# Kernel tuning notes

Measured on AMD Instinct MI355X. Metric: run time of the kernel, lower is better.

Reference implementation:

```python
import jax, jax.numpy as jnp
import numpy as np

D_MODEL = 1024
NUM_HEADS = 16
D_K = D_MODEL // NUM_HEADS
THETA = 10000.0


def _apply_rope(x, positions):
    # x: [B, H, S, d_k], positions: [B, S]
    dk = x.shape[-1]
    freq = 1.0 / (THETA ** (jnp.arange(0, dk, 2, dtype=jnp.float32) / dk))  # [dk/2]
    ang = positions.astype(jnp.float32)[:, None, :, None] * freq  # [B,1,S,dk/2]
    cos, sin = jnp.cos(ang), jnp.sin(ang)
    x_even = x[..., 0::2]
    x_odd = x[..., 1::2]
    re = x_even * cos - x_odd * sin
    ro = x_even * sin + x_odd * cos
    # interleave back: [..., dk/2, 2] -> [..., dk]
    return jnp.stack([re, ro], axis=-1).reshape(x.shape)


def setup_inputs() -> dict:
    key = jax.random.key(0)
    kx, kq, kk, kv, ko = jax.random.split(key, 5)
    B, S = 2, 2048
    std = (2.0 / (D_MODEL + D_MODEL)) ** 0.5
    x = jax.random.normal(kx, (B, S, D_MODEL), dtype=jnp.float32)
    Wq = jax.random.normal(kq, (D_MODEL, D_MODEL), dtype=jnp.float32) * std
    Wk = jax.random.normal(kk, (D_MODEL, D_MODEL), dtype=jnp.float32) * std
    Wv = jax.random.normal(kv, (D_MODEL, D_MODEL), dtype=jnp.float32) * std
    Wo = jax.random.normal(ko, (D_MODEL, D_MODEL), dtype=jnp.float32) * std
    token_positions = jnp.tile(jnp.arange(S, dtype=jnp.int32)[None, :], (B, 1))
    return {"x": x, "Wq": Wq, "Wk": Wk, "Wv": Wv, "Wo": Wo,
            "token_positions": token_positions}


def reference(x, Wq, Wk, Wv, Wo, token_positions):
    B, S, D = x.shape
    H, dk = NUM_HEADS, D_K
    scale = 1.0 / np.sqrt(dk)
    # Linear is y = x @ W.T with W:[d_out, d_in]
    q = jnp.einsum('bsd,ed->bse', x, Wq).reshape(B, S, H, dk).transpose(0, 2, 1, 3)
    k = jnp.einsum('bsd,ed->bse', x, Wk).reshape(B, S, H, dk).transpose(0, 2, 1, 3)
    v = jnp.einsum('bsd,ed->bse', x, Wv).reshape(B, S, H, dk).transpose(0, 2, 1, 3)
    q = _apply_rope(q, token_positions)
    k = _apply_rope(k, token_positions)
    scores = jnp.einsum('bhqd,bhkd->bhqk', q, k) * scale  # [B,H,S,S]
    causal = jnp.tril(jnp.ones((S, S), dtype=bool))
    scores = jnp.where(causal[None, None, :, :], scores, -jnp.inf)
    probs = jax.nn.softmax(scores, axis=-1)
    attn = jnp.einsum('bhqk,bhkd->bhqd', probs, v)  # [B,H,S,dk]
    attn = attn.transpose(0, 2, 1, 3).reshape(B, S, D)
    return jnp.einsum('bsd,ed->bse', attn, Wo)
```

## Files before the change

kernel.cpp:

```cpp
#include <hip/hip_runtime.h>
#include <hip/hip_bf16.h>
#include <math.h>

#define B_  2
#define S_  2048
#define H_  16
#define D_  1024
#define DK_ 64

typedef __attribute__((ext_vector_type(8))) short bf16x8;
typedef __attribute__((ext_vector_type(8))) unsigned short ushort8v;
typedef __attribute__((ext_vector_type(4))) float f32x4;

__device__ __forceinline__ unsigned short f2bf(float f) {
  unsigned u = __float_as_uint(f);
  unsigned r = (u + 0x7FFFu + ((u >> 16) & 1u)) >> 16;
  return (unsigned short)r;
}
__device__ __forceinline__ unsigned pack_trunc(float lo, float hi) {
  return (__float_as_uint(lo) >> 16) | (__float_as_uint(hi) & 0xffff0000u);
}
__device__ __forceinline__ float fast_exp2(float x) {
#if __has_builtin(__builtin_amdgcn_exp2f)
  return __builtin_amdgcn_exp2f(x);
#else
  return __expf(x * 0.69314718056f);
#endif
}
__device__ __forceinline__ void gload_lds16(const unsigned short* g,
                                            unsigned short* l) {
  __builtin_amdgcn_global_load_lds(
      (const __attribute__((address_space(1))) unsigned int*)(const void*)g,
      (__attribute__((address_space(3))) unsigned int*)(void*)l, 16, 0, 0);
}

__global__ __launch_bounds__(256)
void cast5_bf16(const float* __restrict__ x,  const float* __restrict__ wq,
                const float* __restrict__ wk, const float* __restrict__ wv,
                const float* __restrict__ wo,
                unsigned short* __restrict__ xb,  unsigned short* __restrict__ wqb,
                unsigned short* __restrict__ wkb, unsigned short* __restrict__ wvb,
                unsigned short* __restrict__ wob)
{
  const int idx = blockIdx.x;
  const float* s; unsigned short* d; int lblk;
  if (idx < 2048) { s = x; d = xb; lblk = idx; }
  else {
    int t = idx - 2048;
    int w = t >> 9;
    lblk  = t & 511;
    s = (w == 0) ? wq  : (w == 1) ? wk  : (w == 2) ? wv  : wo;
    d = (w == 0) ? wqb : (w == 1) ? wkb : (w == 2) ? wvb : wob;
  }
  size_t i0 = ((size_t)lblk * 256 + threadIdx.x) * 8;
  float4 v0 = *(const float4*)(s + i0);
  float4 v1 = *(const float4*)(s + i0 + 4);
  ushort8v o;
  o[0] = f2bf(v0.x); o[1] = f2bf(v0.y); o[2] = f2bf(v0.z); o[3] = f2bf(v0.w);
  o[4] = f2bf(v1.x); o[5] = f2bf(v1.y); o[6] = f2bf(v1.z); o[7] = f2bf(v1.w);
  *(ushort8v*)(d + i0) = o;
}

__global__ __launch_bounds__(256)
void gemm_qkv(const unsigned short* __restrict__ A0,
              const unsigned short* __restrict__ W0,
              const unsigned short* __restrict__ W1,
              const unsigned short* __restrict__ W2,
              unsigned short* __restrict__ qh,
              unsigned short* __restrict__ kh,
              unsigned short* __restrict__ vt,
              const int* __restrict__ tp)
{
  const int z = blockIdx.z;

  __shared__ unsigned short As[128 * 32];
  __shared__ unsigned short Bs[128 * 32];
  __shared__ int tps[128];

  const int tid   = threadIdx.x;
  const int wave  = tid >> 6;
  const int lane  = tid & 63;
  const int quad  = lane >> 4;
  const int col16 = lane & 15;
  const int wr    = (wave >> 1) * 64;
  const int wc    = (wave & 1) * 64;

  const int row0 = (z == 2) ? blockIdx.x * 128 : blockIdx.y * 128;
  const int col0 = (z == 2) ? blockIdx.y * 128 : blockIdx.x * 128;
  const unsigned short* Aptr = (z == 0) ? A0 : (z == 1) ? A0 : W2;
  const unsigned short* Bptr = (z == 0) ? W0 : (z == 1) ? W1 : A0;

  if (z < 2 && tid < 128) tps[tid] = tp[row0 + tid];

  const int srow = wave * 16 + (lane >> 2);
  const int scol = ((lane & 3) ^ ((lane >> 2) & 3)) * 8;
  const unsigned short* gA = Aptr + (size_t)(row0 + srow) * D_ + scol;
  const unsigned short* gB = Bptr + (size_t)(col0 + srow) * D_ + scol;
  unsigned short* lA0 = &As[(wave * 16) * 32];
  unsigned short* lA1 = &As[(wave * 16 + 64) * 32];
  unsigned short* lB0 = &Bs[(wave * 16) * 32];
  unsigned short* lB1 = &Bs[(wave * 16 + 64) * 32];

  f32x4 acc[4][4];
  #pragma unroll
  for (int mt = 0; mt < 4; ++mt)
    #pragma unroll
    for (int nt = 0; nt < 4; ++nt)
      #pragma unroll
      for (int r = 0; r < 4; ++r) acc[mt][nt][r] = 0.f;

  const int jx = (quad ^ (col16 & 3)) * 8;

  for (int k0 = 0; k0 < D_; k0 += 32) {
    __syncthreads();
    gload_lds16(gA + k0,                   lA0);
    gload_lds16(gA + (size_t)64 * D_ + k0, lA1);
    gload_lds16(gB + k0,                   lB0);
    gload_lds16(gB + (size_t)64 * D_ + k0, lB1);
    __syncthreads();

    bf16x8 af[4], bfr[4];
    #pragma unroll
    for (int mt = 0; mt < 4; ++mt)
      af[mt] = *(const bf16x8*)&As[(wr + mt * 16 + col16) * 32 + jx];
    #pragma unroll
    for (int nt = 0; nt < 4; ++nt)
      bfr[nt] = *(const bf16x8*)&Bs[(wc + nt * 16 + col16) * 32 + jx];

    #pragma unroll
    for (int mt = 0; mt < 4; ++mt)
      #pragma unroll
      for (int nt = 0; nt < 4; ++nt)
        acc[mt][nt] = __builtin_amdgcn_mfma_f32_16x16x32_bf16(
            af[mt], bfr[nt], acc[mt][nt], 0, 0, 0);
  }

  if (z == 2) {
    #pragma unroll
    for (int mt = 0; mt < 4; ++mt)
      #pragma unroll
      for (int r = 0; r < 4; ++r) {
        int c = row0 + wr + mt * 16 + quad * 4 + r;
        int h = c >> 6, d = c & 63;
        #pragma unroll
        for (int nt = 0; nt < 4; ++nt) {
          int t  = col0 + wc + nt * 16 + col16;
          int bb = t >> 11, sl = t & (S_ - 1);
          vt[((size_t)((bb << 4) + h) * DK_ + d) * S_ + sl] =
              f2bf(acc[mt][nt][r]);
        }
      }
  } else {
    unsigned short* C = z ? kh : qh;
    const float qs = z ? 1.0f : 0.1803368801111204f;
    const float sgn = (col16 & 1) ? 1.f : -1.f;
    float freqr[4];
    #pragma unroll
    for (int nt = 0; nt < 4; ++nt) {
      int i = ((wc + nt * 16 + col16) & 63) >> 1;
      freqr[nt] = exp2f(-0.4152410118f * (float)i);
    }
    #pragma unroll
    for (int mt = 0; mt < 4; ++mt)
      #pragma unroll
      for (int r = 0; r < 4; ++r) {
        int rl  = wr + mt * 16 + quad * 4 + r;
        int row = row0 + rl;
        float p = (float)tps[rl];
        #pragma unroll
        for (int nt = 0; nt < 4; ++nt) {
          int col = col0 + wc + nt * 16 + col16;
          float ang = p * freqr[nt];
          float sn = __sinf(ang), cs = __cosf(ang);
          float val = acc[mt][nt][r];
          float oth = __shfl_xor(val, 1);
          C[(size_t)row * D_ + col] = f2bf((val * cs + oth * sgn * sn) * qs);
        }
      }
  }
}

__global__ __launch_bounds__(256)
void gemm_wo(const unsigned short* __restrict__ A,
             const unsigned short* __restrict__ W,
             float* __restrict__ C)
{
  __shared__ unsigned short As[64 * 32];
  __shared__ unsigned short Bs[128 * 32];

  const int tid   = threadIdx.x;
  const int wave  = tid >> 6;
  const int lane  = tid & 63;
  const int quad  = lane >> 4;
  const int col16 = lane & 15;
  const int row0  = blockIdx.y * 64;
  const int col0  = blockIdx.x * 128;
  const int wr    = (wave >> 1) * 32;
  const int wc    = (wave & 1) * 64;

  const int srow = wave * 16 + (lane >> 2);
  const int scol = ((lane & 3) ^ ((lane >> 2) & 3)) * 8;
  const unsigned short* gA = A + (size_t)(row0 + srow) * D_ + scol;
  const unsigned short* gB = W + (size_t)(col0 + srow) * D_ + scol;
  unsigned short* lA0 = &As[(wave * 16) * 32];
  unsigned short* lB0 = &Bs[(wave * 16) * 32];
  unsigned short* lB1 = &Bs[(wave * 16 + 64) * 32];

  f32x4 acc[2][4];
  #pragma unroll
  for (int mt = 0; mt < 2; ++mt)
    #pragma unroll
    for (int nt = 0; nt < 4; ++nt)
      #pragma unroll
      for (int r = 0; r < 4; ++r) acc[mt][nt][r] = 0.f;

  const int jx = (quad ^ (col16 & 3)) * 8;

  for (int k0 = 0; k0 < D_; k0 += 32) {
    __syncthreads();
    gload_lds16(gA + k0,                   lA0);
    gload_lds16(gB + k0,                   lB0);
    gload_lds16(gB + (size_t)64 * D_ + k0, lB1);
    __syncthreads();

    bf16x8 af[2], bfr[4];
    #pragma unroll
    for (int mt = 0; mt < 2; ++mt)
      af[mt] = *(const bf16x8*)&As[(wr + mt * 16 + col16) * 32 + jx];
    #pragma unroll
    for (int nt = 0; nt < 4; ++nt)
      bfr[nt] = *(const bf16x8*)&Bs[(wc + nt * 16 + col16) * 32 + jx];

    #pragma unroll
    for (int mt = 0; mt < 2; ++mt)
      #pragma unroll
      for (int nt = 0; nt < 4; ++nt)
        acc[mt][nt] = __builtin_amdgcn_mfma_f32_16x16x32_bf16(
            af[mt], bfr[nt], acc[mt][nt], 0, 0, 0);
  }

  #pragma unroll
  for (int mt = 0; mt < 2; ++mt)
    #pragma unroll
    for (int r = 0; r < 4; ++r) {
      int row = row0 + wr + mt * 16 + quad * 4 + r;
      #pragma unroll
      for (int nt = 0; nt < 4; ++nt) {
        int col = col0 + wc + nt * 16 + col16;
        C[(size_t)row * D_ + col] = acc[mt][nt][r];
      }
    }
}

__device__ __forceinline__ void attn_side(
    const unsigned short* __restrict__ Ks, const unsigned short* __restrict__ Vs,
    unsigned short (* __restrict__ Pl)[72],
    const bf16x8* qf, f32x4* Oacc, float& l_i,
    int quad, int col, int qlocal, bool diag)
{
  const int jx = quad ^ (col & 7);
  f32x4 st[4];
  #pragma unroll
  for (int nb = 0; nb < 4; ++nb) {
    const int s0 = (nb * 16 + col) * 8 + jx;
    bf16x8 ka0 = *(const bf16x8*)(Ks + s0 * 8);
    bf16x8 ka1 = *(const bf16x8*)(Ks + (s0 ^ 4) * 8);
    f32x4 a = {-24.f, -24.f, -24.f, -24.f};
    a = __builtin_amdgcn_mfma_f32_16x16x32_bf16(ka0, qf[0], a, 0, 0, 0);
    a = __builtin_amdgcn_mfma_f32_16x16x32_bf16(ka1, qf[1], a, 0, 0, 0);
    st[nb] = a;
  }

  if (diag) {
    #pragma unroll
    for (int nb = 0; nb < 4; ++nb)
      #pragma unroll
      for (int r = 0; r < 4; ++r)
        if (nb * 16 + quad * 4 + r > qlocal) st[nb][r] = -1e30f;
  }

  float rsum = 0.f;
  #pragma unroll
  for (int nb = 0; nb < 4; ++nb)
    #pragma unroll
    for (int r = 0; r < 4; ++r) {
      float pv = fast_exp2(st[nb][r]);
      st[nb][r] = pv;
      rsum += pv;
    }
  rsum += __shfl_xor(rsum, 16);
  rsum += __shfl_xor(rsum, 32);
  l_i += rsum;

  #pragma unroll
  for (int nb = 0; nb < 4; ++nb) {
    uint2 pk;
    pk.x = pack_trunc(st[nb][0], st[nb][1]);
    pk.y = pack_trunc(st[nb][2], st[nb][3]);
    *(uint2*)&Pl[col][nb * 16 + quad * 4] = pk;
  }

  bf16x8 pf0 = *(const bf16x8*)&Pl[col][quad * 8];
  bf16x8 pf1 = *(const bf16x8*)&Pl[col][32 + quad * 8];
  #pragma unroll
  for (int nb = 0; nb < 4; ++nb) {
    const int s0 = (nb * 16 + col) * 8 + jx;
    bf16x8 va0 = *(const bf16x8*)(Vs + s0 * 8);
    bf16x8 va1 = *(const bf16x8*)(Vs + (s0 ^ 4) * 8);
    Oacc[nb] = __builtin_amdgcn_mfma_f32_16x16x32_bf16(va0, pf0, Oacc[nb], 0, 0, 0);
    Oacc[nb] = __builtin_amdgcn_mfma_f32_16x16x32_bf16(va1, pf1, Oacc[nb], 0, 0, 0);
  }
}

__global__ __launch_bounds__(256)
void attn_mfma(const unsigned short* __restrict__ Q,
               const unsigned short* __restrict__ K,
               const unsigned short* __restrict__ Vt,
               unsigned short* __restrict__ O)
{
  const int qtA  = blockIdx.x;
  const int qtB  = 31 - qtA;
  const int bh   = blockIdx.y;
  const int b    = bh >> 4, h = bh & 15;
  const int tid  = threadIdx.x;
  const int wave = tid >> 6;
  const int lane = tid & 63;
  const int quad = lane >> 4;
  const int col  = lane & 15;
  const int qlocal = wave * 16 + col;

  __shared__ unsigned short Ks[1024 * 8];
  __shared__ unsigned short Vs[1024 * 8];
  __shared__ unsigned short PlA[4][16][72];
  __shared__ unsigned short PlB[4][16][72];

  const size_t qkbase = (size_t)b * S_ * D_ + (size_t)h * DK_;
  const size_t vtbase = (size_t)bh * DK_ * S_;

  const int qrowA = qtA * 64 + qlocal;
  const int qrowB = qtB * 64 + qlocal;
  bf16x8 qfA[2], qfB[2];
  qfA[0] = *(const bf16x8*)(Q + qkbase + (size_t)qrowA * D_ + quad * 8);
  qfA[1] = *(const bf16x8*)(Q + qkbase + (size_t)qrowA * D_ + 32 + quad * 8);
  qfB[0] = *(const bf16x8*)(Q + qkbase + (size_t)qrowB * D_ + quad * 8);
  qfB[1] = *(const bf16x8*)(Q + qkbase + (size_t)qrowB * D_ + 32 + quad * 8);

  const int sr = tid >> 3;
  const int sj = (tid & 7) ^ (sr & 7);
  const unsigned short* gK = K + qkbase + (size_t)sr * D_ + sj * 8;
  const unsigned short* gV = Vt + vtbase + (size_t)sr * S_ + sj * 8;

  f32x4 OaccA[4], OaccB[4];
  #pragma unroll
  for (int nb = 0; nb < 4; ++nb)
    #pragma unroll
    for (int r = 0; r < 4; ++r) { OaccA[nb][r] = 0.f; OaccB[nb][r] = 0.f; }
  float lA = 0.f, lB = 0.f;

  const int nK128 = (qtB + 2) >> 1;

  for (int m = 0; m < nK128; ++m) {
    __syncthreads();
    #pragma unroll
    for (int half = 0; half < 2; ++half) {
      const int kbase = m * 128 + half * 64;
      #pragma unroll
      for (int p = 0; p < 2; ++p) {
        gload_lds16(gK + (size_t)(kbase + p * 32) * D_,
                    &Ks[(size_t)half * 4096 + (size_t)(p * 256 + wave * 64) * 8]);
        gload_lds16(gV + (size_t)(p * 32) * S_ + kbase,
                    &Vs[(size_t)half * 4096 + (size_t)(p * 256 + wave * 64) * 8]);
      }
    }
    __syncthreads();

    #pragma unroll
    for (int half = 0; half < 2; ++half) {
      const int g = 2 * m + half;
      const unsigned short* KsH = Ks + half * 4096;
      const unsigned short* VsH = Vs + half * 4096;
      if (g <= qtB)
        attn_side(KsH, VsH, PlB[wave], qfB, OaccB, lB, quad, col, qlocal,
                  g == qtB);
      if (g <= qtA)
        attn_side(KsH, VsH, PlA[wave], qfA, OaccA, lA, quad, col, qlocal,
                  g == qtA);
    }
  }

  const float invA = 1.0f / lA;
  const float invB = 1.0f / lB;
  #pragma unroll
  for (int nb = 0; nb < 4; ++nb) {
    int d = nb * 16 + quad * 4;
    ushort4 oa, ob;
    oa.x = f2bf(OaccA[nb][0] * invA); oa.y = f2bf(OaccA[nb][1] * invA);
    oa.z = f2bf(OaccA[nb][2] * invA); oa.w = f2bf(OaccA[nb][3] * invA);
    ob.x = f2bf(OaccB[nb][0] * invB); ob.y = f2bf(OaccB[nb][1] * invB);
    ob.z = f2bf(OaccB[nb][2] * invB); ob.w = f2bf(OaccB[nb][3] * invB);
    *(ushort4*)(O + (size_t)b * S_ * D_ + (size_t)qrowA * D_ + h * DK_ + d) = oa;
    *(ushort4*)(O + (size_t)b * S_ * D_ + (size_t)qrowB * D_ + h * DK_ + d) = ob;
  }
}

extern "C" void kernel_launch(void* const* d_in, const int* in_sizes, int n_in,
                              void* d_out, int out_size, void* d_ws, size_t ws_size,
                              hipStream_t stream)
{
  const float* x  = (const float*)d_in[0];
  const float* Wq = (const float*)d_in[1];
  const float* Wk = (const float*)d_in[2];
  const float* Wv = (const float*)d_in[3];
  const float* Wo = (const float*)d_in[4];
  const int*   tp = (const int*)d_in[5];
  float* out = (float*)d_out;

  const size_t NTOK = (size_t)B_ * S_ * D_;
  const size_t NW   = (size_t)D_ * D_;
  unsigned short* qh  = (unsigned short*)d_ws;
  unsigned short* kh  = qh + NTOK;
  unsigned short* vt  = kh + NTOK;
  unsigned short* xb  = vt + NTOK;
  unsigned short* wqb = xb + NTOK;
  unsigned short* wkb = wqb + NW;
  unsigned short* wvb = wkb + NW;
  unsigned short* wob = wvb + NW;
  unsigned short* ab  = xb;

  cast5_bf16<<<dim3(4096), 256, 0, stream>>>(
      x, Wq, Wk, Wv, Wo, xb, wqb, wkb, wvb, wob);

  gemm_qkv<<<dim3(D_ / 128, (B_ * S_) / 128, 3), 256, 0, stream>>>(
      xb, wqb, wkb, wvb, qh, kh, vt, tp);

  attn_mfma<<<dim3(16, B_ * H_), 256, 0, stream>>>(qh, kh, vt, ab);

  gemm_wo<<<dim3(D_ / 128, (B_ * S_) / 64), 256, 0, stream>>>(ab, wob, out);
}
```

Measured before the change: 192.4 us.

## Double-buffer LDS tiles in GEMM and attention loops, MFMA softmax row sums

The QKV GEMM, output GEMM and attention kernels now use two LDS buffers. Each loop prefetches the next K tile into the alternate buffer after one barrier per step, so the global-to-LDS copy overlaps the MFMA work on the current tile, and the second barrier is gone. The attention loop now steps through 64-key tiles instead of 128-key pairs. The softmax denominator is computed with an MFMA of the bf16 probability tile against a ones vector, replacing the per-lane adds and cross-lane shuffles. This uses more LDS in the GEMMs, which may reduce occupancy, and the row sum now uses bf16-rounded probabilities, which matches the numerator.

```diff
diff --git a/kernel.cpp b/kernel.cpp
--- a/kernel.cpp
+++ b/kernel.cpp
@@ -73,8 +73,8 @@
 {
   const int z = blockIdx.z;
 
-  __shared__ unsigned short As[128 * 32];
-  __shared__ unsigned short Bs[128 * 32];
+  __shared__ unsigned short As[2 * 128 * 32];
+  __shared__ unsigned short Bs[2 * 128 * 32];
   __shared__ int tps[128];
 
   const int tid   = threadIdx.x;
@@ -87,7 +87,7 @@
 
   const int row0 = (z == 2) ? blockIdx.x * 128 : blockIdx.y * 128;
   const int col0 = (z == 2) ? blockIdx.y * 128 : blockIdx.x * 128;
-  const unsigned short* Aptr = (z == 0) ? A0 : (z == 1) ? A0 : W2;
+  const unsigned short* Aptr = (z == 2) ? W2 : A0;
   const unsigned short* Bptr = (z == 0) ? W0 : (z == 1) ? W1 : A0;
 
   if (z < 2 && tid < 128) tps[tid] = tp[row0 + tid];
@@ -96,10 +96,15 @@
   const int scol = ((lane & 3) ^ ((lane >> 2) & 3)) * 8;
   const unsigned short* gA = Aptr + (size_t)(row0 + srow) * D_ + scol;
   const unsigned short* gB = Bptr + (size_t)(col0 + srow) * D_ + scol;
-  unsigned short* lA0 = &As[(wave * 16) * 32];
-  unsigned short* lA1 = &As[(wave * 16 + 64) * 32];
-  unsigned short* lB0 = &Bs[(wave * 16) * 32];
-  unsigned short* lB1 = &Bs[(wave * 16 + 64) * 32];
+
+  auto stage = [&](int k0, int buf) {
+    unsigned short* a = As + buf * 4096;
+    unsigned short* b = Bs + buf * 4096;
+    gload_lds16(gA + k0,                   a + (wave * 16) * 32);
+    gload_lds16(gA + (size_t)64 * D_ + k0, a + (wave * 16 + 64) * 32);
+    gload_lds16(gB + k0,                   b + (wave * 16) * 32);
+    gload_lds16(gB + (size_t)64 * D_ + k0, b + (wave * 16 + 64) * 32);
+  };
 
   f32x4 acc[4][4];
   #pragma unroll
@@ -111,21 +116,21 @@
 
   const int jx = (quad ^ (col16 & 3)) * 8;
 
+  stage(0, 0);
   for (int k0 = 0; k0 < D_; k0 += 32) {
+    const int buf = (k0 >> 5) & 1;
     __syncthreads();
-    gload_lds16(gA + k0,                   lA0);
-    gload_lds16(gA + (size_t)64 * D_ + k0, lA1);
-    gload_lds16(gB + k0,                   lB0);
-    gload_lds16(gB + (size_t)64 * D_ + k0, lB1);
-    __syncthreads();
-
+    if (k0 + 32 < D_) stage(k0 + 32, buf ^ 1);
+
+    const unsigned short* a = As + buf * 4096;
+    const unsigned short* b = Bs + buf * 4096;
     bf16x8 af[4], bfr[4];
     #pragma unroll
     for (int mt = 0; mt < 4; ++mt)
-      af[mt] = *(const bf16x8*)&As[(wr + mt * 16 + col16) * 32 + jx];
+      af[mt] = *(const bf16x8*)&a[(wr + mt * 16 + col16) * 32 + jx];
     #pragma unroll
     for (int nt = 0; nt < 4; ++nt)
-      bfr[nt] = *(const bf16x8*)&Bs[(wc + nt * 16 + col16) * 32 + jx];
+      bfr[nt] = *(const bf16x8*)&b[(wc + nt * 16 + col16) * 32 + jx];
 
     #pragma unroll
     for (int mt = 0; mt < 4; ++mt)
@@ -185,8 +190,8 @@
              const unsigned short* __restrict__ W,
              float* __restrict__ C)
 {
-  __shared__ unsigned short As[64 * 32];
-  __shared__ unsigned short Bs[128 * 32];
+  __shared__ unsigned short As[2 * 64 * 32];
+  __shared__ unsigned short Bs[2 * 128 * 32];
 
   const int tid   = threadIdx.x;
   const int wave  = tid >> 6;
@@ -202,9 +207,14 @@
   const int scol = ((lane & 3) ^ ((lane >> 2) & 3)) * 8;
   const unsigned short* gA = A + (size_t)(row0 + srow) * D_ + scol;
   const unsigned short* gB = W + (size_t)(col0 + srow) * D_ + scol;
-  unsigned short* lA0 = &As[(wave * 16) * 32];
-  unsigned short* lB0 = &Bs[(wave * 16) * 32];
-  unsigned short* lB1 = &Bs[(wave * 16 + 64) * 32];
+
+  auto stage = [&](int k0, int buf) {
+    unsigned short* a = As + buf * 2048;
+    unsigned short* b = Bs + buf * 4096;
+    gload_lds16(gA + k0,                   a + (wave * 16) * 32);
+    gload_lds16(gB + k0,                   b + (wave * 16) * 32);
+    gload_lds16(gB + (size_t)64 * D_ + k0, b + (wave * 16 + 64) * 32);
+  };
 
   f32x4 acc[2][4];
   #pragma unroll
@@ -216,20 +226,21 @@
 
   const int jx = (quad ^ (col16 & 3)) * 8;
 
+  stage(0, 0);
   for (int k0 = 0; k0 < D_; k0 += 32) {
+    const int buf = (k0 >> 5) & 1;
     __syncthreads();
-    gload_lds16(gA + k0,                   lA0);
-    gload_lds16(gB + k0,                   lB0);
-    gload_lds16(gB + (size_t)64 * D_ + k0, lB1);
-    __syncthreads();
-
+    if (k0 + 32 < D_) stage(k0 + 32, buf ^ 1);
+
+    const unsigned short* a = As + buf * 2048;
+    const unsigned short* b = Bs + buf * 4096;
     bf16x8 af[2], bfr[4];
     #pragma unroll
     for (int mt = 0; mt < 2; ++mt)
-      af[mt] = *(const bf16x8*)&As[(wr + mt * 16 + col16) * 32 + jx];
+      af[mt] = *(const bf16x8*)&a[(wr + mt * 16 + col16) * 32 + jx];
     #pragma unroll
     for (int nt = 0; nt < 4; ++nt)
-      bfr[nt] = *(const bf16x8*)&Bs[(wc + nt * 16 + col16) * 32 + jx];
+      bfr[nt] = *(const bf16x8*)&b[(wc + nt * 16 + col16) * 32 + jx];
 
     #pragma unroll
     for (int mt = 0; mt < 2; ++mt)
@@ -258,6 +269,9 @@
     const bf16x8* qf, f32x4* Oacc, float& l_i,
     int quad, int col, int qlocal, bool diag)
 {
+  const short ONE = (short)0x3F80;
+  const bf16x8 ones = {ONE, ONE, ONE, ONE, ONE, ONE, ONE, ONE};
+
   const int jx = quad ^ (col & 7);
   f32x4 st[4];
   #pragma unroll
@@ -279,18 +293,10 @@
         if (nb * 16 + quad * 4 + r > qlocal) st[nb][r] = -1e30f;
   }
 
-  float rsum = 0.f;
   #pragma unroll
   for (int nb = 0; nb < 4; ++nb)
     #pragma unroll
-    for (int r = 0; r < 4; ++r) {
-      float pv = fast_exp2(st[nb][r]);
-      st[nb][r] = pv;
-      rsum += pv;
-    }
-  rsum += __shfl_xor(rsum, 16);
-  rsum += __shfl_xor(rsum, 32);
-  l_i += rsum;
+    for (int r = 0; r < 4; ++r) st[nb][r] = fast_exp2(st[nb][r]);
 
   #pragma unroll
   for (int nb = 0; nb < 4; ++nb) {
@@ -302,6 +308,12 @@
 
   bf16x8 pf0 = *(const bf16x8*)&Pl[col][quad * 8];
   bf16x8 pf1 = *(const bf16x8*)&Pl[col][32 + quad * 8];
+
+  f32x4 lacc = {0.f, 0.f, 0.f, 0.f};
+  lacc = __builtin_amdgcn_mfma_f32_16x16x32_bf16(ones, pf0, lacc, 0, 0, 0);
+  lacc = __builtin_amdgcn_mfma_f32_16x16x32_bf16(ones, pf1, lacc, 0, 0, 0);
+  l_i += lacc[0];
+
   #pragma unroll
   for (int nb = 0; nb < 4; ++nb) {
     const int s0 = (nb * 16 + col) * 8 + jx;
@@ -329,8 +341,8 @@
   const int col  = lane & 15;
   const int qlocal = wave * 16 + col;
 
-  __shared__ unsigned short Ks[1024 * 8];
-  __shared__ unsigned short Vs[1024 * 8];
+  __shared__ unsigned short Ks[2 * 512 * 8];
+  __shared__ unsigned short Vs[2 * 512 * 8];
   __shared__ unsigned short PlA[4][16][72];
   __shared__ unsigned short PlB[4][16][72];
 
@@ -350,6 +362,17 @@
   const unsigned short* gK = K + qkbase + (size_t)sr * D_ + sj * 8;
   const unsigned short* gV = Vt + vtbase + (size_t)sr * S_ + sj * 8;
 
+  auto stage = [&](int g, int buf) {
+    const int kbase = g * 64;
+    #pragma unroll
+    for (int p = 0; p < 2; ++p) {
+      gload_lds16(gK + (size_t)(kbase + p * 32) * D_,
+                  &Ks[buf * 4096 + (p * 256 + wave * 64) * 8]);
+      gload_lds16(gV + (size_t)(p * 32) * S_ + kbase,
+                  &Vs[buf * 4096 + (p * 256 + wave * 64) * 8]);
+    }
+  };
+
   f32x4 OaccA[4], OaccB[4];
   #pragma unroll
   for (int nb = 0; nb < 4; ++nb)
@@ -357,35 +380,19 @@
     for (int r = 0; r < 4; ++r) { OaccA[nb][r] = 0.f; OaccB[nb][r] = 0.f; }
   float lA = 0.f, lB = 0.f;
 
-  const int nK128 = (qtB + 2) >> 1;
-
-  for (int m = 0; m < nK128; ++m) {
+  stage(0, 0);
+  for (int g = 0; g <= qtB; ++g) {
+    const int buf = g & 1;
     __syncthreads();
-    #pragma unroll
-    for (int half = 0; half < 2; ++half) {
-      const int kbase = m * 128 + half * 64;
-      #pragma unroll
-      for (int p = 0; p < 2; ++p) {
-        gload_lds16(gK + (size_t)(kbase + p * 32) * D_,
-                    &Ks[(size_t)half * 4096 + (size_t)(p * 256 + wave * 64) * 8]);
-        gload_lds16(gV + (size_t)(p * 32) * S_ + kbase,
-                    &Vs[(size_t)half * 4096 + (size_t)(p * 256 + wave * 64) * 8]);
-      }
-    }
-    __syncthreads();
-
-    #pragma unroll
-    for (int half = 0; half < 2; ++half) {
-      const int g = 2 * m + half;
-      const unsigned short* KsH = Ks + half * 4096;
-      const unsigned short* VsH = Vs + half * 4096;
-      if (g <= qtB)
-        attn_side(KsH, VsH, PlB[wave], qfB, OaccB, lB, quad, col, qlocal,
-                  g == qtB);
-      if (g <= qtA)
-        attn_side(KsH, VsH, PlA[wave], qfA, OaccA, lA, quad, col, qlocal,
-                  g == qtA);
-    }
+    if (g < qtB) stage(g + 1, buf ^ 1);
+
+    const unsigned short* KsH = Ks + buf * 4096;
+    const unsigned short* VsH = Vs + buf * 4096;
+    attn_side(KsH, VsH, PlB[wave], qfB, OaccB, lB, quad, col, qlocal,
+              g == qtB);
+    if (g <= qtA)
+      attn_side(KsH, VsH, PlA[wave], qfA, OaccA, lA, quad, col, qlocal,
+                g == qtA);
   }
 
   const float invA = 1.0f / lA;
```

Result: faster. 185.9 us (-3.4%).
